# Kernel tuning notes

Hardware: AMD Instinct MI355X
Metric: run time of the kernel (lower is better)

## Reference

```python
import jax, jax.numpy as jnp
import numpy as np

N_NODES = 50000
N_EDGES = 800000
D_FEAT = 128
EMBED = 128
HEADS = 8
HEAD_DIM = EMBED // HEADS


def setup_inputs() -> dict:
    key = jax.random.key(0)
    ks = jax.random.split(key, 10)
    xavier = jax.nn.initializers.xavier_normal()
    return {
        "nodes": jax.random.normal(ks[0], (N_NODES, D_FEAT), jnp.float32),
        "edges": jax.random.normal(ks[1], (N_EDGES, D_FEAT), jnp.float32),
        "senders": jax.random.randint(ks[2], (N_EDGES,), 0, N_NODES, jnp.int32),
        "receivers": jax.random.randint(ks[3], (N_EDGES,), 0, N_NODES, jnp.int32),
        "Ws_k": xavier(ks[4], (D_FEAT, EMBED), jnp.float32),
        "Ws_b": jnp.zeros((EMBED,), jnp.float32),
        "Wr_k": xavier(ks[5], (D_FEAT, EMBED), jnp.float32),
        "Wr_b": jnp.zeros((EMBED,), jnp.float32),
        "We_k": xavier(ks[6], (D_FEAT, EMBED), jnp.float32),
        "We_b": jnp.zeros((EMBED,), jnp.float32),
        "a": xavier(ks[7], (HEADS, HEAD_DIM), jnp.float32),
    }


def reference(nodes, edges, senders, receivers, Ws_k, Ws_b, Wr_k, Wr_b, We_k, We_b, a):
    N = nodes.shape[0]
    E = edges.shape[0]
    H, D = a.shape
    # Node-level projections (linear, so equivalent to projecting gathered edge endpoints)
    hs = nodes @ Ws_k + Ws_b            # [N, HD]  (W_s on sent attributes)
    hr = nodes @ Wr_k + Wr_b            # [N, HD]  (W_r on received attributes)
    he = edges @ We_k + We_b            # [E, HD]  (W_e on edge attributes)
    sent = hs[senders]                  # [E, HD]
    x = jax.nn.leaky_relu(sent + hr[receivers] + he)  # default slope 0.01, as original
    xh = x.reshape(E, H, D)
    logits = jnp.sum(xh * a, axis=-1)   # [E, H]
    # segment_softmax over receivers (stable: subtract per-segment max)
    mx = jax.ops.segment_max(logits, receivers, num_segments=N)  # [N, H]
    mx = jnp.where(jnp.isfinite(mx), mx, 0.0)
    ex = jnp.exp(logits - mx[receivers])                         # [E, H]
    denom = jax.ops.segment_sum(ex, receivers, num_segments=N)   # [N, H]
    w = ex / denom[receivers]                                    # [E, H]
    msg = (w[..., None] * sent.reshape(E, H, D)).reshape(E, H * D)
    out = jax.ops.segment_sum(msg, receivers, num_segments=N)    # [N, HD]
    return out
```

## Files before the change

kernel.cpp:

```cpp
#include <hip/hip_runtime.h>

#define N_NODES 50000
#define N_EDGES 800000
#define D 128
#define HEADS 8

typedef __attribute__((ext_vector_type(8))) short short8b;
typedef __attribute__((ext_vector_type(8))) unsigned short ushort8v;
typedef __attribute__((ext_vector_type(4))) float f32x4;

__device__ __forceinline__ unsigned short f2bf_rne(float f) {
    unsigned int u = __float_as_uint(f);
    u += 0x7FFFu + ((u >> 16) & 1u);
    return (unsigned short)(u >> 16);
}
__device__ __forceinline__ float bf2f(unsigned short u) {
    return __uint_as_float(((unsigned int)u) << 16);
}

template <int CTRL>
__device__ __forceinline__ float dpp_radd(float v) {
    int s = __builtin_amdgcn_update_dpp(0, __float_as_int(v), CTRL, 0xF, 0xF, true);
    return v + __int_as_float(s);
}
__device__ __forceinline__ float rowsum16(float v) {
    v = dpp_radd<0xB1>(v);
    v = dpp_radd<0x4E>(v);
    v = dpp_radd<0x141>(v);
    v = dpp_radd<0x140>(v);
    return v;
}

#define K1_ROWS 256
__global__ __launch_bounds__(256, 3) void k_node_proj_mfma(
    const float* __restrict__ nodes,
    const float* __restrict__ Ws, const float* __restrict__ bs,
    const float* __restrict__ Wr, const float* __restrict__ br,
    unsigned short* __restrict__ hsb, unsigned short* __restrict__ hrb)
{
    __shared__ __align__(16) unsigned short WT[D][136];
    __shared__ __align__(16) unsigned short At[64][136];
    const int ntiles = (N_NODES + K1_ROWS - 1) / K1_ROWS;
    int bx = blockIdx.x;
    int proj = (bx >= ntiles) ? 1 : 0;
    int tile = proj ? (bx - ntiles) : bx;
    const float* W    = proj ? Wr : Ws;
    const float* bias = proj ? br : bs;
    unsigned short* outp = proj ? hrb : hsb;
    int t = threadIdx.x;
    int lane = t & 63;
    int wv = t >> 6;
    int lg = lane >> 4;
    int li = lane & 15;

    #pragma unroll 8
    for (int j = 0; j < 64; ++j) {
        int idx = t + 256 * j;
        int k = idx >> 7, c = idx & 127;
        WT[c][k] = f2bf_rne(W[idx]);
    }
    float b_ct[8];
    #pragma unroll
    for (int ct = 0; ct < 8; ++ct) b_ct[ct] = bias[ct * 16 + li];

    #pragma unroll 1
    for (int sub = 0; sub < 4; ++sub) {
        int row0 = tile * K1_ROWS + sub * 64;
        if (row0 >= N_NODES) break;
        __syncthreads();
        {
            const float4* Nv = (const float4*)nodes;
            #pragma unroll
            for (int j = 0; j < 8; ++j) {
                int fi = t + 256 * j;
                int r = row0 + (fi >> 5);
                float4 v = make_float4(0.f, 0.f, 0.f, 0.f);
                if (r < N_NODES) v = Nv[(size_t)r * 32 + (fi & 31)];
                ushort4 b;
                b.x = f2bf_rne(v.x); b.y = f2bf_rne(v.y);
                b.z = f2bf_rne(v.z); b.w = f2bf_rne(v.w);
                *(ushort4*)&At[fi >> 5][(fi & 31) * 4] = b;
            }
        }
        __syncthreads();

        short8b afr[4];
        #pragma unroll
        for (int kb = 0; kb < 4; ++kb)
            afr[kb] = *(const short8b*)&At[wv * 16 + li][kb * 32 + lg * 8];

        f32x4 accs[8];
        #pragma unroll
        for (int ct = 0; ct < 8; ++ct) {
            f32x4 acc = {0.f, 0.f, 0.f, 0.f};
            #pragma unroll
            for (int kb = 0; kb < 4; ++kb) {
                short8b bfr = *(const short8b*)&WT[ct * 16 + li][kb * 32 + lg * 8];
                acc = __builtin_amdgcn_mfma_f32_16x16x32_bf16(afr[kb], bfr, acc, 0, 0, 0);
            }
            accs[ct] = acc;
        }
        #pragma unroll
        for (int j = 0; j < 4; ++j) {
            int r = row0 + wv * 16 + lg * 4 + j;
            if (r < N_NODES) {
                uint4 w;
                w.x = (unsigned)f2bf_rne(accs[0][j] + b_ct[0])
                    | ((unsigned)f2bf_rne(accs[1][j] + b_ct[1]) << 16);
                w.y = (unsigned)f2bf_rne(accs[2][j] + b_ct[2])
                    | ((unsigned)f2bf_rne(accs[3][j] + b_ct[3]) << 16);
                w.z = (unsigned)f2bf_rne(accs[4][j] + b_ct[4])
                    | ((unsigned)f2bf_rne(accs[5][j] + b_ct[5]) << 16);
                w.w = (unsigned)f2bf_rne(accs[6][j] + b_ct[6])
                    | ((unsigned)f2bf_rne(accs[7][j] + b_ct[7]) << 16);
                *(uint4*)&outp[(size_t)r * D + li * 8] = w;
            }
        }
    }
}

__global__ __launch_bounds__(256) void k_hist(
    const int* __restrict__ receivers, int* __restrict__ deg)
{
    int i = blockIdx.x * 256 + threadIdx.x;
    if (i < N_EDGES) atomicAdd(&deg[receivers[i]], 1);
}

#define SCAN_CHUNK 49
__global__ __launch_bounds__(1024) void k_scan(
    const int* __restrict__ deg, int* __restrict__ rowptr, int* __restrict__ cursor)
{
    __shared__ int sm[1024];
    int t = threadIdx.x;
    int base = t * SCAN_CHUNK;
    int lsum = 0;
    #pragma unroll 4
    for (int i = 0; i < SCAN_CHUNK; ++i) {
        int idx = base + i;
        if (idx < N_NODES) lsum += deg[idx];
    }
    sm[t] = lsum;
    __syncthreads();
    for (int off = 1; off < 1024; off <<= 1) {
        int v = (t >= off) ? sm[t - off] : 0;
        __syncthreads();
        sm[t] += v;
        __syncthreads();
    }
    int run = (t > 0) ? sm[t - 1] : 0;
    for (int i = 0; i < SCAN_CHUNK; ++i) {
        int idx = base + i;
        if (idx < N_NODES) {
            rowptr[idx] = run;
            cursor[idx] = run;
            run += deg[idx];
        }
    }
    if (t == 1023) rowptr[N_NODES] = sm[1023];
}

__global__ __launch_bounds__(256) void k_fill(
    const int* __restrict__ receivers, const int* __restrict__ senders,
    int* __restrict__ cursor,
    int* __restrict__ eids, int* __restrict__ s_csr, int* __restrict__ r_csr)
{
    int i = blockIdx.x * 256 + threadIdx.x;
    if (i < N_EDGES) {
        int r = receivers[i];
        int pos = atomicAdd(&cursor[r], 1);
        eids[pos]  = i;
        s_csr[pos] = senders[i];
        r_csr[pos] = r;
    }
}

#define BLK_E 64
__global__ __launch_bounds__(256, 3) void k_edge_logits_mfma(
    const float* __restrict__ edges,
    const int* __restrict__ eids, const int* __restrict__ s_csr,
    const int* __restrict__ r_csr,
    const float* __restrict__ We, const float* __restrict__ be,
    const float* __restrict__ a,
    const unsigned short* __restrict__ hsb, const unsigned short* __restrict__ hrb,
    float* __restrict__ ex)
{
    __shared__ __align__(16) unsigned short WeT[D][136];
    __shared__ __align__(16) unsigned short Et[BLK_E][136];
    int t = threadIdx.x;
    int lane = t & 63;
    int wv = t >> 6;
    int lg = lane >> 4;
    int li = lane & 15;

    #pragma unroll 8
    for (int j = 0; j < 64; ++j) {
        int idx = t + 256 * j;
        int k = idx >> 7, c = idx & 127;
        WeT[c][k] = f2bf_rne(We[idx]);
    }
    float a_h[HEADS], be_h[HEADS];
    #pragma unroll
    for (int h = 0; h < HEADS; ++h) {
        a_h[h]  = a[h * 16 + li];
        be_h[h] = be[h * 16 + li];
    }
    __syncthreads();

    const int ntiles = N_EDGES / BLK_E;
    for (int tile = blockIdx.x; tile < ntiles; tile += gridDim.x) {
        int pbase = tile * BLK_E + wv * 16;

        {
            const float4* Ev = (const float4*)edges;
            #pragma unroll
            for (int j = 0; j < 8; ++j) {
                int fi = lane + 64 * j;
                int rloc = fi >> 5;
                int e = eids[pbase + rloc];
                float4 v = Ev[(size_t)e * 32 + (fi & 31)];
                ushort4 b;
                b.x = f2bf_rne(v.x); b.y = f2bf_rne(v.y);
                b.z = f2bf_rne(v.z); b.w = f2bf_rne(v.w);
                *(ushort4*)&Et[wv * 16 + rloc][(fi & 31) * 4] = b;
            }
        }

        int sj[4], rj[4];
        #pragma unroll
        for (int j = 0; j < 4; ++j) {
            sj[j] = s_csr[pbase + lg * 4 + j];
            rj[j] = r_csr[pbase + lg * 4 + j];
        }
        ushort8v g_hs[4], g_hr[4];
        #pragma unroll
        for (int j = 0; j < 4; ++j) {
            g_hs[j] = *(const ushort8v*)(hsb + (size_t)sj[j] * D + li * 8);
            g_hr[j] = *(const ushort8v*)(hrb + (size_t)rj[j] * D + li * 8);
        }

        asm volatile("s_waitcnt lgkmcnt(0)" ::: "memory");
        __builtin_amdgcn_sched_barrier(0);

        short8b afr[4];
        #pragma unroll
        for (int kb = 0; kb < 4; ++kb)
            afr[kb] = *(const short8b*)&Et[wv * 16 + li][kb * 32 + lg * 8];

        float hold[8];
        #pragma unroll
        for (int h = 0; h < HEADS; ++h) {
            f32x4 acc = {0.f, 0.f, 0.f, 0.f};
            #pragma unroll
            for (int kb = 0; kb < 4; ++kb) {
                short8b bfr = *(const short8b*)&WeT[h * 16 + li][kb * 32 + lg * 8];
                acc = __builtin_amdgcn_mfma_f32_16x16x32_bf16(afr[kb], bfr, acc, 0, 0, 0);
            }
            float pr[4];
            #pragma unroll
            for (int j = 0; j < 4; ++j) {
                float x = acc[j] + be_h[h] + bf2f(g_hs[j][h]) + bf2f(g_hr[j][h]);
                x = fmaxf(x, 0.01f * x);
                pr[j] = rowsum16(x * a_h[h]);
            }
            float qa = (li & 4) ? pr[1] : pr[0];
            float qb = (li & 4) ? pr[3] : pr[2];
            hold[h] = __expf((li & 8) ? qb : qa);
        }
        {
            float a0 = (li & 1) ? hold[2] : hold[0];
            float a1 = (li & 1) ? hold[6] : hold[4];
            float ea = (li & 2) ? a1 : a0;
            float b0 = (li & 1) ? hold[3] : hold[1];
            float b1 = (li & 1) ? hold[7] : hold[5];
            float eb = (li & 2) ? b1 : b0;
            int h1 = 2 * (li & 3);
            int o  = 4 * lg + (li >> 2);
            *(float2*)&ex[(size_t)(pbase + o) * HEADS + h1] = make_float2(ea, eb);
        }
        __builtin_amdgcn_wave_barrier();
    }
}

__global__ __launch_bounds__(256) void k_gather_out(
    const int* __restrict__ rowptr, const int* __restrict__ s_csr,
    const unsigned short* __restrict__ hsb, const float* __restrict__ ex,
    float* __restrict__ out)
{
    __shared__ float obuf[4][128];
    int wvid = threadIdx.x >> 6;
    int r = blockIdx.x * 4 + wvid;
    int l = threadIdx.x & 63;
    int h1 = 2 * (l & 3);
    int c1 = (l >> 2) + 16 * h1;
    int beg = rowptr[r], end = rowptr[r + 1];

    float2 acc = make_float2(0.f, 0.f);
    float ds1 = 0.f, ds2 = 0.f;
    for (int j0 = beg; j0 < end; j0 += 16) {
        int cnt = end - j0;
        int s[16]; float2 w2[16];
        #pragma unroll
        for (int q = 0; q < 16; ++q)
            if (q < cnt) {
                s[q]  = s_csr[j0 + q];
                w2[q] = *(const float2*)&ex[(size_t)(j0 + q) * HEADS + h1];
            }
        #pragma unroll
        for (int q = 0; q < 16; ++q)
            if (q < cnt) {
                ushort2 hv = *(const ushort2*)&hsb[(size_t)s[q] * D + 2 * l];
                acc.x += w2[q].x * bf2f(hv.x);
                acc.y += w2[q].y * bf2f(hv.y);
                ds1   += w2[q].x;
                ds2   += w2[q].y;
            }
    }
    float i1 = (end > beg && ds1 != 0.f) ? (1.0f / ds1) : 0.f;
    float i2 = (end > beg && ds2 != 0.f) ? (1.0f / ds2) : 0.f;
    obuf[wvid][c1]      = acc.x * i1;
    obuf[wvid][c1 + 16] = acc.y * i2;
    asm volatile("s_waitcnt lgkmcnt(0)" ::: "memory");
    __builtin_amdgcn_sched_barrier(0);
    float2 o2 = *(const float2*)&obuf[wvid][2 * l];
    *(float2*)&out[(size_t)r * D + 2 * l] = o2;
}

extern "C" void kernel_launch(void* const* d_in, const int* in_sizes, int n_in,
                              void* d_out, int out_size, void* d_ws, size_t ws_size,
                              hipStream_t stream) {
    const float* nodes     = (const float*)d_in[0];
    const float* edges     = (const float*)d_in[1];
    const int*   senders   = (const int*)d_in[2];
    const int*   receivers = (const int*)d_in[3];
    const float* Ws = (const float*)d_in[4];
    const float* bs = (const float*)d_in[5];
    const float* Wr = (const float*)d_in[6];
    const float* br = (const float*)d_in[7];
    const float* We = (const float*)d_in[8];
    const float* be = (const float*)d_in[9];
    const float* a  = (const float*)d_in[10];
    float* out = (float*)d_out;

    unsigned short* hsb = (unsigned short*)d_ws;
    unsigned short* hrb = hsb + (size_t)N_NODES * D;
    float* ex   = (float*)(hrb + (size_t)N_NODES * D);
    int* deg    = (int*)(ex + (size_t)N_EDGES * HEADS);
    int* rowptr = deg + N_NODES;
    int* cursor = rowptr + N_NODES + 1;
    int* eids   = cursor + N_NODES;
    int* s_csr  = eids + N_EDGES;
    int* r_csr  = s_csr + N_EDGES;

    (void)hipMemsetAsync(deg, 0, N_NODES * sizeof(int), stream);
    k_hist<<<N_EDGES / 256, 256, 0, stream>>>(receivers, deg);
    k_scan<<<1, 1024, 0, stream>>>(deg, rowptr, cursor);
    k_fill<<<N_EDGES / 256, 256, 0, stream>>>(receivers, senders, cursor,
                                              eids, s_csr, r_csr);
    int ntiles_n = (N_NODES + K1_ROWS - 1) / K1_ROWS;
    k_node_proj_mfma<<<ntiles_n * 2, 256, 0, stream>>>(nodes, Ws, bs, Wr, br, hsb, hrb);
    k_edge_logits_mfma<<<2048, 256, 0, stream>>>(edges, eids, s_csr, r_csr,
                                                 We, be, a, hsb, hrb, ex);
    k_gather_out<<<N_NODES / 4, 256, 0, stream>>>(rowptr, s_csr, hsb, ex, out);
}
```

Measured before the change: 483.9 us.

## Fuse edge-logit and aggregation kernels into a per-receiver attention kernel

Replaces the edge-tiled logit kernel and the separate gather kernel with one kernel that walks each receiver's CSR segment. It computes logits, exponentials, denominators and weighted sums in registers, then normalizes once per node. The goal is to drop the per-edge ex buffer write and reread, the r_csr array, and the per-edge hr gather, since hr is loaded once per node. In exchange, every one of the many non-persistent blocks reloads and converts the full We matrix into shared memory. Partial 16-edge tiles waste MFMA work on low-degree nodes.

```diff
diff --git a/kernel.cpp b/kernel.cpp
--- a/kernel.cpp
+++ b/kernel.cpp
@@ -162,7 +162,7 @@
 __global__ __launch_bounds__(256) void k_fill(
     const int* __restrict__ receivers, const int* __restrict__ senders,
     int* __restrict__ cursor,
-    int* __restrict__ eids, int* __restrict__ s_csr, int* __restrict__ r_csr)
+    int* __restrict__ eids, int* __restrict__ s_csr)
 {
     int i = blockIdx.x * 256 + threadIdx.x;
     if (i < N_EDGES) {
@@ -170,22 +170,21 @@
         int pos = atomicAdd(&cursor[r], 1);
         eids[pos]  = i;
         s_csr[pos] = senders[i];
-        r_csr[pos] = r;
-    }
-}
-
-#define BLK_E 64
-__global__ __launch_bounds__(256, 3) void k_edge_logits_mfma(
+    }
+}
+
+__global__ __launch_bounds__(256, 3) void k_fused_attn(
     const float* __restrict__ edges,
-    const int* __restrict__ eids, const int* __restrict__ s_csr,
-    const int* __restrict__ r_csr,
+    const int* __restrict__ rowptr, const int* __restrict__ eids,
+    const int* __restrict__ s_csr,
     const float* __restrict__ We, const float* __restrict__ be,
     const float* __restrict__ a,
     const unsigned short* __restrict__ hsb, const unsigned short* __restrict__ hrb,
-    float* __restrict__ ex)
+    float* __restrict__ out)
 {
     __shared__ __align__(16) unsigned short WeT[D][136];
-    __shared__ __align__(16) unsigned short Et[BLK_E][136];
+    __shared__ __align__(16) unsigned short Et[64][136];
+    __shared__ float obuf[4][128];
     int t = threadIdx.x;
     int lane = t & 63;
     int wv = t >> 6;
@@ -206,9 +205,17 @@
     }
     __syncthreads();
 
-    const int ntiles = N_EDGES / BLK_E;
-    for (int tile = blockIdx.x; tile < ntiles; tile += gridDim.x) {
-        int pbase = tile * BLK_E + wv * 16;
+    int node = blockIdx.x * 4 + wv;
+    int beg = rowptr[node], end = rowptr[node + 1];
+
+    ushort8v g_hr = *(const ushort8v*)(hrb + (size_t)node * D + li * 8);
+
+    float den[8], oac[8];
+    #pragma unroll
+    for (int h = 0; h < HEADS; ++h) { den[h] = 0.f; oac[h] = 0.f; }
+
+    for (int j0 = beg; j0 < end; j0 += 16) {
+        int cnt = end - j0;
 
         {
             const float4* Ev = (const float4*)edges;
@@ -216,27 +223,27 @@
             for (int j = 0; j < 8; ++j) {
                 int fi = lane + 64 * j;
                 int rloc = fi >> 5;
-                int e = eids[pbase + rloc];
-                float4 v = Ev[(size_t)e * 32 + (fi & 31)];
-                ushort4 b;
-                b.x = f2bf_rne(v.x); b.y = f2bf_rne(v.y);
-                b.z = f2bf_rne(v.z); b.w = f2bf_rne(v.w);
-                *(ushort4*)&Et[wv * 16 + rloc][(fi & 31) * 4] = b;
-            }
-        }
-
-        int sj[4], rj[4];
+                if (rloc < cnt) {
+                    int e = eids[j0 + rloc];
+                    float4 v = Ev[(size_t)e * 32 + (fi & 31)];
+                    ushort4 b;
+                    b.x = f2bf_rne(v.x); b.y = f2bf_rne(v.y);
+                    b.z = f2bf_rne(v.z); b.w = f2bf_rne(v.w);
+                    *(ushort4*)&Et[wv * 16 + rloc][(fi & 31) * 4] = b;
+                }
+            }
+        }
+
+        int sj[4];
         #pragma unroll
         for (int j = 0; j < 4; ++j) {
-            sj[j] = s_csr[pbase + lg * 4 + j];
-            rj[j] = r_csr[pbase + lg * 4 + j];
-        }
-        ushort8v g_hs[4], g_hr[4];
-        #pragma unroll
-        for (int j = 0; j < 4; ++j) {
+            int p = j0 + lg * 4 + j;
+            sj[j] = s_csr[p < end ? p : (end - 1)];
+        }
+        ushort8v g_hs[4];
+        #pragma unroll
+        for (int j = 0; j < 4; ++j)
             g_hs[j] = *(const ushort8v*)(hsb + (size_t)sj[j] * D + li * 8);
-            g_hr[j] = *(const ushort8v*)(hrb + (size_t)rj[j] * D + li * 8);
-        }
 
         asm volatile("s_waitcnt lgkmcnt(0)" ::: "memory");
         __builtin_amdgcn_sched_barrier(0);
@@ -246,7 +253,6 @@
         for (int kb = 0; kb < 4; ++kb)
             afr[kb] = *(const short8b*)&Et[wv * 16 + li][kb * 32 + lg * 8];
 
-        float hold[8];
         #pragma unroll
         for (int h = 0; h < HEADS; ++h) {
             f32x4 acc = {0.f, 0.f, 0.f, 0.f};
@@ -255,74 +261,37 @@
                 short8b bfr = *(const short8b*)&WeT[h * 16 + li][kb * 32 + lg * 8];
                 acc = __builtin_amdgcn_mfma_f32_16x16x32_bf16(afr[kb], bfr, acc, 0, 0, 0);
             }
-            float pr[4];
             #pragma unroll
             for (int j = 0; j < 4; ++j) {
-                float x = acc[j] + be_h[h] + bf2f(g_hs[j][h]) + bf2f(g_hr[j][h]);
+                float x = acc[j] + be_h[h] + bf2f(g_hs[j][h]) + bf2f(g_hr[h]);
                 x = fmaxf(x, 0.01f * x);
-                pr[j] = rowsum16(x * a_h[h]);
-            }
-            float qa = (li & 4) ? pr[1] : pr[0];
-            float qb = (li & 4) ? pr[3] : pr[2];
-            hold[h] = __expf((li & 8) ? qb : qa);
-        }
-        {
-            float a0 = (li & 1) ? hold[2] : hold[0];
-            float a1 = (li & 1) ? hold[6] : hold[4];
-            float ea = (li & 2) ? a1 : a0;
-            float b0 = (li & 1) ? hold[3] : hold[1];
-            float b1 = (li & 1) ? hold[7] : hold[5];
-            float eb = (li & 2) ? b1 : b0;
-            int h1 = 2 * (li & 3);
-            int o  = 4 * lg + (li >> 2);
-            *(float2*)&ex[(size_t)(pbase + o) * HEADS + h1] = make_float2(ea, eb);
+                float pr = rowsum16(x * a_h[h]);
+                bool valid = (lg * 4 + j) < cnt;
+                float e_ = valid ? __expf(pr) : 0.f;
+                den[h] += e_;
+                oac[h] += e_ * bf2f(g_hs[j][h]);
+            }
         }
         __builtin_amdgcn_wave_barrier();
     }
-}
-
-__global__ __launch_bounds__(256) void k_gather_out(
-    const int* __restrict__ rowptr, const int* __restrict__ s_csr,
-    const unsigned short* __restrict__ hsb, const float* __restrict__ ex,
-    float* __restrict__ out)
-{
-    __shared__ float obuf[4][128];
-    int wvid = threadIdx.x >> 6;
-    int r = blockIdx.x * 4 + wvid;
-    int l = threadIdx.x & 63;
-    int h1 = 2 * (l & 3);
-    int c1 = (l >> 2) + 16 * h1;
-    int beg = rowptr[r], end = rowptr[r + 1];
-
-    float2 acc = make_float2(0.f, 0.f);
-    float ds1 = 0.f, ds2 = 0.f;
-    for (int j0 = beg; j0 < end; j0 += 16) {
-        int cnt = end - j0;
-        int s[16]; float2 w2[16];
-        #pragma unroll
-        for (int q = 0; q < 16; ++q)
-            if (q < cnt) {
-                s[q]  = s_csr[j0 + q];
-                w2[q] = *(const float2*)&ex[(size_t)(j0 + q) * HEADS + h1];
-            }
-        #pragma unroll
-        for (int q = 0; q < 16; ++q)
-            if (q < cnt) {
-                ushort2 hv = *(const ushort2*)&hsb[(size_t)s[q] * D + 2 * l];
-                acc.x += w2[q].x * bf2f(hv.x);
-                acc.y += w2[q].y * bf2f(hv.y);
-                ds1   += w2[q].x;
-                ds2   += w2[q].y;
-            }
-    }
-    float i1 = (end > beg && ds1 != 0.f) ? (1.0f / ds1) : 0.f;
-    float i2 = (end > beg && ds2 != 0.f) ? (1.0f / ds2) : 0.f;
-    obuf[wvid][c1]      = acc.x * i1;
-    obuf[wvid][c1 + 16] = acc.y * i2;
+
+    float wn[8];
+    #pragma unroll
+    for (int h = 0; h < HEADS; ++h) {
+        float d = den[h];
+        d += __shfl_xor(d, 16); d += __shfl_xor(d, 32);
+        float o = oac[h];
+        o += __shfl_xor(o, 16); o += __shfl_xor(o, 32);
+        wn[h] = (end > beg && d != 0.f) ? (o / d) : 0.f;
+    }
+    float wa = (lg == 0) ? wn[0] : (lg == 1) ? wn[2] : (lg == 2) ? wn[4] : wn[6];
+    float wb = (lg == 0) ? wn[1] : (lg == 1) ? wn[3] : (lg == 2) ? wn[5] : wn[7];
+    obuf[wv][32 * lg + li]      = wa;
+    obuf[wv][32 * lg + 16 + li] = wb;
     asm volatile("s_waitcnt lgkmcnt(0)" ::: "memory");
     __builtin_amdgcn_sched_barrier(0);
-    float2 o2 = *(const float2*)&obuf[wvid][2 * l];
-    *(float2*)&out[(size_t)r * D + 2 * l] = o2;
+    float2 o2 = *(const float2*)&obuf[wv][2 * lane];
+    *(float2*)&out[(size_t)node * D + 2 * lane] = o2;
 }
 
 extern "C" void kernel_launch(void* const* d_in, const int* in_sizes, int n_in,
@@ -343,22 +312,19 @@
 
     unsigned short* hsb = (unsigned short*)d_ws;
     unsigned short* hrb = hsb + (size_t)N_NODES * D;
-    float* ex   = (float*)(hrb + (size_t)N_NODES * D);
-    int* deg    = (int*)(ex + (size_t)N_EDGES * HEADS);
+    int* deg    = (int*)(hrb + (size_t)N_NODES * D);
     int* rowptr = deg + N_NODES;
     int* cursor = rowptr + N_NODES + 1;
     int* eids   = cursor + N_NODES;
     int* s_csr  = eids + N_EDGES;
-    int* r_csr  = s_csr + N_EDGES;
 
     (void)hipMemsetAsync(deg, 0, N_NODES * sizeof(int), stream);
     k_hist<<<N_EDGES / 256, 256, 0, stream>>>(receivers, deg);
     k_scan<<<1, 1024, 0, stream>>>(deg, rowptr, cursor);
     k_fill<<<N_EDGES / 256, 256, 0, stream>>>(receivers, senders, cursor,
-                                              eids, s_csr, r_csr);
+                                              eids, s_csr);
     int ntiles_n = (N_NODES + K1_ROWS - 1) / K1_ROWS;
     k_node_proj_mfma<<<ntiles_n * 2, 256, 0, stream>>>(nodes, Ws, bs, Wr, br, hsb, hrb);
-    k_edge_logits_mfma<<<2048, 256, 0, stream>>>(edges, eids, s_csr, r_csr,
-                                                 We, be, a, hsb, hrb, ex);
-    k_gather_out<<<N_NODES / 4, 256, 0, stream>>>(rowptr, s_csr, hsb, ex, out);
-}
+    k_fused_attn<<<N_NODES / 4, 256, 0, stream>>>(edges, rowptr, eids, s_csr,
+                                                  We, be, a, hsb, hrb, out);
+}
```

Measured after the change: 692.2 us. 43.0% more time.
